# Optimization experiments

Hardware: AMD Instinct MI355X
Metric: run time of the kernel (lower is better)

## Reference

```python
import jax, jax.numpy as jnp
import numpy as np

N, E = 50000, 400000
IN_CH, HID, HEADS, EDGE_DIM = 128, 64, 4, 3
NEG_SLOPE = 0.2


def gatv2_conv(x, src, dst, edge_attr, Wl, Wr, We, att, bias):
    # x: [N, F_in]; Wl/Wr: [H*C, F_in]; We: [H*C, edge_dim]; att: [H, C]; bias: [C]
    H, C = att.shape
    n = x.shape[0]
    xl = (x @ Wl.T).reshape(n, H, C)   # source-side transform (lin_l)
    xr = (x @ Wr.T).reshape(n, H, C)   # target-side transform (lin_r)
    e = (edge_attr @ We.T).reshape(-1, H, C)
    z = jax.nn.leaky_relu(xl[src] + xr[dst] + e, NEG_SLOPE)  # [E,H,C]
    alpha = jnp.einsum('ehc,hc->eh', z, att)                 # [E,H]
    # segment softmax over incoming edges per destination node
    amax = jax.ops.segment_max(alpha, dst, num_segments=n)
    alpha = jnp.exp(alpha - amax[dst])
    denom = jax.ops.segment_sum(alpha, dst, num_segments=n)
    alpha = alpha / (denom[dst] + 1e-16)
    msg = xl[src] * alpha[:, :, None]                        # [E,H,C]
    out = jax.ops.segment_sum(msg, dst, num_segments=n)      # [N,H,C]
    return out.mean(axis=1) + bias                           # concat=False -> head mean


def setup_inputs() -> dict:
    key = jax.random.key(0)
    ks = jax.random.split(key, 16)
    s = 0.1
    return {
        'x': jax.random.normal(ks[0], (N, IN_CH), jnp.float32),
        'edge_index': jax.random.randint(ks[1], (2, E), 0, N, jnp.int32),
        'edge_attr': jax.random.normal(ks[2], (E, EDGE_DIM), jnp.float32),
        'Wl1': jax.random.normal(ks[3], (HEADS * HID, IN_CH), jnp.float32) * s,
        'Wr1': jax.random.normal(ks[4], (HEADS * HID, IN_CH), jnp.float32) * s,
        'We1': jax.random.normal(ks[5], (HEADS * HID, EDGE_DIM), jnp.float32) * s,
        'att1': jax.random.normal(ks[6], (HEADS, HID), jnp.float32) * s,
        'b1': jnp.zeros((HID,), jnp.float32),
        'Wl2': jax.random.normal(ks[7], (HEADS * HID, HID), jnp.float32) * s,
        'Wr2': jax.random.normal(ks[8], (HEADS * HID, HID), jnp.float32) * s,
        'We2': jax.random.normal(ks[9], (HEADS * HID, EDGE_DIM), jnp.float32) * s,
        'att2': jax.random.normal(ks[10], (HEADS, HID), jnp.float32) * s,
        'b2': jnp.zeros((HID,), jnp.float32),
        'prelu_w': jnp.full((HID,), 0.25, jnp.float32),
    }


def reference(x, edge_index, edge_attr, Wl1, Wr1, We1, att1, b1, Wl2, Wr2, We2, att2, b2, prelu_w):
    src, dst = edge_index[0], edge_index[1]
    h = gatv2_conv(x, src, dst, edge_attr, Wl1, Wr1, We1, att1, b1)
    h = gatv2_conv(h, src, dst, edge_attr, Wl2, Wr2, We2, att2, b2)
    return jnp.where(h >= 0, h, prelu_w * h)  # PReLU, per-channel weight
```

## Files before the change

kernel.cpp:

```cpp
#include <hip/hip_runtime.h>
#include <hip/hip_bf16.h>

#define HC 256

typedef __attribute__((ext_vector_type(8))) short bf16x8;
typedef __attribute__((ext_vector_type(4))) float f32x4;
typedef __attribute__((ext_vector_type(2))) float f32x2;

__device__ __forceinline__ void gl_lds16(const void* g, void* l) {
  __builtin_amdgcn_global_load_lds(
      (const __attribute__((address_space(1))) unsigned int*)g,
      (__attribute__((address_space(3))) unsigned int*)l, 16, 0, 0);
}

__device__ __forceinline__ void cast_w_one(const float* Wl, const float* Wr,
                                           ushort* WT, int F, int idx) {
  int col = idx / F, f = idx - col * F;
  float v = (col < 256) ? Wl[col * F + f] : Wr[(col - 256) * F + f];
  __hip_bfloat16 h = __float2bfloat16(v);
  WT[(size_t)col * F + f] = *(ushort*)&h;
}

__global__ void k_weights_deg(const float* __restrict__ Wl1, const float* __restrict__ Wr1,
                              ushort* __restrict__ WT1, const float* __restrict__ Wl2,
                              const float* __restrict__ Wr2, ushort* __restrict__ WT2,
                              int* __restrict__ deg, int n) {
  int idx = blockIdx.x * blockDim.x + threadIdx.x;
  const int t1 = 512 * 128, t2 = 512 * 64;
  if (idx < t1) {
    cast_w_one(Wl1, Wr1, WT1, 128, idx);
  } else if (idx < t1 + t2) {
    cast_w_one(Wl2, Wr2, WT2, 64, idx - t1);
  } else if (idx < t1 + t2 + n) {
    deg[idx - t1 - t2] = 0;
  }
}

template <int F>
__global__ __launch_bounds__(256) void gemm_mfma(const ushort* __restrict__ A,
                                                 const ushort* __restrict__ WT,
                                                 ushort* __restrict__ xlb,
                                                 ushort* __restrict__ xrb, int n_nodes) {
  constexpr int NSTEP = F / 64;
  __shared__ __align__(16) ushort As[128 * 64];
  __shared__ __align__(16) ushort Bs[128 * 64];
  const int tid = threadIdx.x;
  const int wv = tid >> 6, lane = tid & 63;
  const int m16 = lane & 15, quad = lane >> 4;
  const int col0 = blockIdx.x * 128;
  const int row0 = blockIdx.y * 128;
  const int wm = (wv >> 1) * 64, wn = (wv & 1) * 64;

  f32x4 acc[4][4];
#pragma unroll
  for (int i = 0; i < 4; ++i)
#pragma unroll
    for (int j = 0; j < 4; ++j) acc[i][j] = (f32x4){0.f, 0.f, 0.f, 0.f};

#pragma unroll
  for (int s = 0; s < NSTEP; ++s) {
    const int khat = s * 64;
    __syncthreads();
#pragma unroll
    for (int t = 0; t < 4; ++t) {
      const int sl16 = tid + 256 * t;
      const int row = sl16 >> 3, sl = sl16 & 7;
      const int gch = sl ^ (row & 7);
      const int grow = row0 + row;
      if (grow < n_nodes)
        gl_lds16(A + (size_t)grow * F + khat + gch * 8, As + sl16 * 8);
      gl_lds16(WT + (size_t)(col0 + row) * F + khat + gch * 8, Bs + sl16 * 8);
    }
    __syncthreads();
#pragma unroll
    for (int kh = 0; kh < 2; ++kh) {
      bf16x8 af[4], bf[4];
#pragma unroll
      for (int i = 0; i < 4; ++i) {
        const int row = wm + i * 16 + m16;
        const int slot = (kh * 4 + quad) ^ (row & 7);
        af[i] = *(bf16x8*)&As[row * 64 + slot * 8];
      }
#pragma unroll
      for (int j = 0; j < 4; ++j) {
        const int col = wn + j * 16 + m16;
        const int slot = (kh * 4 + quad) ^ (col & 7);
        bf[j] = *(bf16x8*)&Bs[col * 64 + slot * 8];
      }
#pragma unroll
      for (int i = 0; i < 4; ++i)
#pragma unroll
        for (int j = 0; j < 4; ++j)
          acc[i][j] =
              __builtin_amdgcn_mfma_f32_16x16x32_bf16(af[i], bf[j], acc[i][j], 0, 0, 0);
    }
  }
  const bool is_xl = (col0 < 256);
#pragma unroll
  for (int i = 0; i < 4; ++i) {
#pragma unroll
    for (int r = 0; r < 4; ++r) {
      const int grow = row0 + wm + i * 16 + quad * 4 + r;
      if (grow < n_nodes) {
#pragma unroll
        for (int j = 0; j < 4; ++j) {
          const float v = acc[i][j][r];
          const int col = col0 + wn + j * 16 + m16;
          __hip_bfloat16 h = __float2bfloat16(v);
          if (is_xl)
            xlb[(size_t)grow * 256 + col] = *(ushort*)&h;
          else
            xrb[(size_t)grow * 256 + (col - 256)] = *(ushort*)&h;
        }
      }
    }
  }
}

__global__ void k_hist(const int* __restrict__ ei, int* __restrict__ deg, int E_) {
  int e = blockIdx.x * blockDim.x + threadIdx.x;
  if (e < E_) atomicAdd(&deg[ei[E_ + e]], 1);
}

__global__ void k_scan_local(const int* __restrict__ deg, int* __restrict__ rowstart,
                             int* __restrict__ partial, int n) {
  __shared__ int a[256], b[256];
  const int t = threadIdx.x;
  const int i = blockIdx.x * 256 + t;
  const int v = (i < n) ? deg[i] : 0;
  a[t] = v;
  __syncthreads();
  int* cur = a;
  int* nxt = b;
  for (int off = 1; off < 256; off <<= 1) {
    int x = cur[t];
    if (t >= off) x += cur[t - off];
    nxt[t] = x;
    __syncthreads();
    int* tmp = cur; cur = nxt; nxt = tmp;
  }
  const int incl = cur[t];
  if (i < n) rowstart[i] = incl - v;
  if (t == 255) partial[blockIdx.x] = incl;
}

__global__ void k_scan_partial(int* __restrict__ partial, int nblk,
                               int* __restrict__ ssrc, float4* __restrict__ sea, int E_) {
  __shared__ int a[256], b[256];
  const int t = threadIdx.x;
  if (t < 8) {
    ssrc[E_ + t] = 0;
    sea[E_ + t] = make_float4(0.f, 0.f, 0.f, 0.f);
  }
  const int v = (t < nblk) ? partial[t] : 0;
  a[t] = v;
  __syncthreads();
  int* cur = a;
  int* nxt = b;
  for (int off = 1; off < 256; off <<= 1) {
    int x = cur[t];
    if (t >= off) x += cur[t - off];
    nxt[t] = x;
    __syncthreads();
    int* tmp = cur; cur = nxt; nxt = tmp;
  }
  if (t < nblk) partial[t] = cur[t] - v;
}

__global__ void k_add_off(int* __restrict__ rowstart, int* __restrict__ cursor,
                          const int* __restrict__ partial, int n, int E_) {
  int i = blockIdx.x * blockDim.x + threadIdx.x;
  if (i < n) {
    int v = rowstart[i] + partial[i >> 8];
    rowstart[i] = v;
    cursor[i] = v;
  }
  if (i == 0) rowstart[n] = E_;
}

__global__ void k_prep(const float* __restrict__ x, ushort* __restrict__ A,
                       const int* __restrict__ ei, const float* __restrict__ ea,
                       int* __restrict__ cursor, int* __restrict__ ssrc,
                       float4* __restrict__ sea, int n, int E_) {
  const int nx8 = n * 16;
  int idx = blockIdx.x * blockDim.x + threadIdx.x;
  if (idx < nx8) {
    const float4* xp = (const float4*)x + (size_t)idx * 2;
    float4 v0 = xp[0], v1 = xp[1];
    float vv[8] = {v0.x, v0.y, v0.z, v0.w, v1.x, v1.y, v1.z, v1.w};
    __align__(16) ushort hb[8];
#pragma unroll
    for (int j = 0; j < 8; ++j) {
      __hip_bfloat16 h = __float2bfloat16(vv[j]);
      hb[j] = *(ushort*)&h;
    }
    *(int4*)(A + (size_t)idx * 8) = *(int4*)hb;
  } else {
    int e = idx - nx8;
    if (e < E_) {
      int dst = ei[E_ + e];
      int pos = atomicAdd(&cursor[dst], 1);
      ssrc[pos] = ei[e];
      sea[pos] = make_float4(ea[e * 3], ea[e * 3 + 1], ea[e * 3 + 2], 0.f);
    }
  }
}

__device__ __forceinline__ f32x2 vmax2(f32x2 a, f32x2 b) {
  return (f32x2){fmaxf(a.x, b.x), fmaxf(a.y, b.y)};
}
__device__ __forceinline__ f32x2 vmin2(f32x2 a, f32x2 b) {
  return (f32x2){fminf(a.x, b.x), fminf(a.y, b.y)};
}

__device__ __forceinline__ void edge_step(
    const ushort4& lu, const float4& eav, const f32x2* we0, const f32x2* we1,
    const f32x2* we2, const f32x2* at, const f32x2* xrl, f32x2& num01,
    f32x2& num23, float& den) {
  f32x2 lav0, lav1;
  lav0.x = __uint_as_float((unsigned)lu.x << 16);
  lav0.y = __uint_as_float((unsigned)lu.y << 16);
  lav1.x = __uint_as_float((unsigned)lu.z << 16);
  lav1.y = __uint_as_float((unsigned)lu.w << 16);
  const f32x2 zero = {0.f, 0.f};
  const f32x2 slope = {0.2f, 0.2f};
  f32x2 pv = zero;
#pragma unroll
  for (int j = 0; j < 2; ++j) {
    f32x2 la = (j == 0) ? lav0 : lav1;
    f32x2 ev = we0[j] * eav.x + we1[j] * eav.y + we2[j] * eav.z;
    f32x2 s = la + xrl[j] + ev;
    f32x2 z = vmax2(s, zero) + slope * vmin2(s, zero);
    pv = pv + z * at[j];
  }
  float p = pv.x + pv.y;
  p += __shfl_xor(p, 1);
  p += __shfl_xor(p, 2);
  p += __shfl_xor(p, 4);
  p += __shfl_xor(p, 8);
  const float w = __expf(p);
  den += w;
  num01 = num01 + (f32x2){w, w} * lav0;
  num23 = num23 + (f32x2){w, w} * lav1;
}

template <int MODE>
__global__ __launch_bounds__(256) void fused_attn(
    const ushort* __restrict__ xlb, const ushort* __restrict__ xrb,
    const int* __restrict__ rowstart, const int* __restrict__ ssrc,
    const float4* __restrict__ sea, const float* __restrict__ We,
    const float* __restrict__ att, const float* __restrict__ bias,
    const float* __restrict__ pw, float* __restrict__ out,
    ushort* __restrict__ outs, int n, int chunk) {
  const int lane = threadIdx.x & 63;
  const int wid =
      __builtin_amdgcn_readfirstlane((blockIdx.x * blockDim.x + threadIdx.x) >> 6);
  const int d0 = wid * chunk;
  if (d0 >= n) return;
  const int d1 = min(d0 + chunk, n);

  f32x2 we0[2], we1[2], we2[2], at[2];
#pragma unroll
  for (int j = 0; j < 4; ++j) {
    int r = 4 * lane + j;
    ((float*)we0)[j] = We[r * 3 + 0];
    ((float*)we1)[j] = We[r * 3 + 1];
    ((float*)we2)[j] = We[r * 3 + 2];
    ((float*)at)[j] = att[r];
  }
  const float4 bias4 = ((const float4*)bias)[lane & 15];
  float4 pw4 = {0.f, 0.f, 0.f, 0.f};
  if (MODE == 1) pw4 = ((const float4*)pw)[lane & 15];
  const ushort4* xlb4 = (const ushort4*)xlb;

  for (int d = d0; d < d1; ++d) {
    const ushort4 xu = ((const ushort4*)xrb)[(unsigned)(d * 64) + lane];
    f32x2 xrl[2];
    xrl[0].x = __uint_as_float((unsigned)xu.x << 16);
    xrl[0].y = __uint_as_float((unsigned)xu.y << 16);
    xrl[1].x = __uint_as_float((unsigned)xu.z << 16);
    xrl[1].y = __uint_as_float((unsigned)xu.w << 16);

    int pos = rowstart[d];
    const int end = rowstart[d + 1];
    f32x2 num01 = {0.f, 0.f}, num23 = {0.f, 0.f};
    float den = 0.f;

    if (pos < end) {
      int s0 = ssrc[pos], s1 = ssrc[pos + 1];
      ushort4 g0 = xlb4[(unsigned)(s0 * 64) + lane];
      ushort4 g1 = xlb4[(unsigned)(s1 * 64) + lane];
      float4 e0 = sea[pos], e1 = sea[pos + 1];
      int sn0 = ssrc[pos + 2], sn1 = ssrc[pos + 3];

      while (pos + 2 <= end) {
        ushort4 h0 = xlb4[(unsigned)(sn0 * 64) + lane];
        ushort4 h1 = xlb4[(unsigned)(sn1 * 64) + lane];
        float4 f0 = sea[pos + 2], f1 = sea[pos + 3];
        sn0 = ssrc[pos + 4];
        sn1 = ssrc[pos + 5];
        edge_step(g0, e0, we0, we1, we2, at, xrl, num01, num23, den);
        edge_step(g1, e1, we0, we1, we2, at, xrl, num01, num23, den);
        g0 = h0; g1 = h1; e0 = f0; e1 = f1;
        pos += 2;
      }
      if (pos < end)
        edge_step(g0, e0, we0, we1, we2, at, xrl, num01, num23, den);
    }

    const float inv = 1.f / (den + 1e-16f);
    float4 r;
    r.x = num01.x * inv;
    r.y = num01.y * inv;
    r.z = num23.x * inv;
    r.w = num23.y * inv;
    r.x += __shfl_xor(r.x, 16);
    r.y += __shfl_xor(r.y, 16);
    r.z += __shfl_xor(r.z, 16);
    r.w += __shfl_xor(r.w, 16);
    r.x += __shfl_xor(r.x, 32);
    r.y += __shfl_xor(r.y, 32);
    r.z += __shfl_xor(r.z, 32);
    r.w += __shfl_xor(r.w, 32);
    if (lane < 16) {
      float o[4];
      o[0] = 0.25f * r.x + bias4.x;
      o[1] = 0.25f * r.y + bias4.y;
      o[2] = 0.25f * r.z + bias4.z;
      o[3] = 0.25f * r.w + bias4.w;
      if (MODE == 1) {
        const float pwv[4] = {pw4.x, pw4.y, pw4.z, pw4.w};
#pragma unroll
        for (int j = 0; j < 4; ++j) o[j] = (o[j] >= 0.f) ? o[j] : pwv[j] * o[j];
        ((float4*)out)[(size_t)d * 16 + lane] = make_float4(o[0], o[1], o[2], o[3]);
      } else {
        ushort hb[4];
#pragma unroll
        for (int j = 0; j < 4; ++j) {
          __hip_bfloat16 h = __float2bfloat16(o[j]);
          hb[j] = *(ushort*)&h;
        }
        *(ushort4*)(outs + (size_t)d * 64 + 4 * lane) =
            make_ushort4(hb[0], hb[1], hb[2], hb[3]);
      }
    }
  }
}

extern "C" void kernel_launch(void* const* d_in, const int* in_sizes, int n_in,
                              void* d_out, int out_size, void* d_ws, size_t ws_size,
                              hipStream_t stream) {
  const float* x    = (const float*)d_in[0];
  const int*   ei   = (const int*)d_in[1];
  const float* ea   = (const float*)d_in[2];
  const float* Wl1  = (const float*)d_in[3];
  const float* Wr1  = (const float*)d_in[4];
  const float* We1  = (const float*)d_in[5];
  const float* att1 = (const float*)d_in[6];
  const float* b1   = (const float*)d_in[7];
  const float* Wl2  = (const float*)d_in[8];
  const float* Wr2  = (const float*)d_in[9];
  const float* We2  = (const float*)d_in[10];
  const float* att2 = (const float*)d_in[11];
  const float* b2   = (const float*)d_in[12];
  const float* pw   = (const float*)d_in[13];
  const int N_ = in_sizes[0] / 128;
  const int E_ = in_sizes[1] / 2;
  float* out = (float*)d_out;

  char* w = (char*)d_ws;
  auto alloc = [&](size_t bytes) {
    char* p = w;
    w += (bytes + 255) & ~size_t(255);
    return p;
  };
  ushort* xlb      = (ushort*)alloc((size_t)N_ * 256 * 2);
  ushort* xrb      = (ushort*)alloc((size_t)N_ * 256 * 2);
  ushort* Ax       = (ushort*)alloc((size_t)N_ * 128 * 2);
  ushort* h2       = (ushort*)alloc((size_t)N_ * 64 * 2);
  int*    ssrc     = (int*)alloc((size_t)(E_ + 8) * 4);
  float4* sea      = (float4*)alloc((size_t)(E_ + 8) * 16);
  int*    deg      = (int*)alloc((size_t)N_ * 4);
  int*    rowstart = (int*)alloc((size_t)(N_ + 1) * 4);
  int*    cursor   = (int*)alloc((size_t)N_ * 4);
  int*    partial  = (int*)alloc(256 * 4);
  ushort* WT1      = (ushort*)alloc((size_t)512 * 128 * 2);
  ushort* WT2      = (ushort*)alloc((size_t)512 * 64 * 2);

  const int wtot = 512 * 128 + 512 * 64 + N_;
  k_weights_deg<<<(wtot + 255) / 256, 256, 0, stream>>>(Wl1, Wr1, WT1, Wl2, Wr2, WT2,
                                                        deg, N_);

  const int nblk = (N_ + 255) / 256;
  k_hist<<<(E_ + 255) / 256, 256, 0, stream>>>(ei, deg, E_);
  k_scan_local<<<nblk, 256, 0, stream>>>(deg, rowstart, partial, N_);
  k_scan_partial<<<1, 256, 0, stream>>>(partial, nblk, ssrc, sea, E_);
  k_add_off<<<nblk, 256, 0, stream>>>(rowstart, cursor, partial, N_, E_);
  const int ptot = N_ * 16 + E_;
  k_prep<<<(ptot + 255) / 256, 256, 0, stream>>>(x, Ax, ei, ea, cursor, ssrc, sea,
                                                 N_, E_);

  const dim3 GG(4, (N_ + 127) / 128);
  const int FW = 8192;
  const int FB = FW / 4;
  const int chunk = (N_ + FW - 1) / FW;

  gemm_mfma<128><<<GG, 256, 0, stream>>>(Ax, WT1, xlb, xrb, N_);
  fused_attn<0><<<FB, 256, 0, stream>>>(xlb, xrb, rowstart, ssrc, sea, We1, att1,
                                        b1, pw, nullptr, h2, N_, chunk);
  gemm_mfma<64><<<GG, 256, 0, stream>>>(h2, WT2, xlb, xrb, N_);
  fused_attn<1><<<FB, 256, 0, stream>>>(xlb, xrb, rowstart, ssrc, sea, We2, att2,
                                        b2, pw, out, nullptr, N_, chunk);
}
```

Baseline: 280.3 us.

## Unroll edge gather to four-way prefetch, fuse histogram into weight cast, shrink node chunk

```diff
diff --git a/kernel.cpp b/kernel.cpp
--- a/kernel.cpp
+++ b/kernel.cpp
@@ -21,18 +21,19 @@
   WT[(size_t)col * F + f] = *(ushort*)&h;
 }
 
-__global__ void k_weights_deg(const float* __restrict__ Wl1, const float* __restrict__ Wr1,
-                              ushort* __restrict__ WT1, const float* __restrict__ Wl2,
-                              const float* __restrict__ Wr2, ushort* __restrict__ WT2,
-                              int* __restrict__ deg, int n) {
+__global__ void k_weights_hist(const float* __restrict__ Wl1, const float* __restrict__ Wr1,
+                               ushort* __restrict__ WT1, const float* __restrict__ Wl2,
+                               const float* __restrict__ Wr2, ushort* __restrict__ WT2,
+                               const int* __restrict__ ei, int* __restrict__ deg, int E_) {
   int idx = blockIdx.x * blockDim.x + threadIdx.x;
   const int t1 = 512 * 128, t2 = 512 * 64;
   if (idx < t1) {
     cast_w_one(Wl1, Wr1, WT1, 128, idx);
   } else if (idx < t1 + t2) {
     cast_w_one(Wl2, Wr2, WT2, 64, idx - t1);
-  } else if (idx < t1 + t2 + n) {
-    deg[idx - t1 - t2] = 0;
+  } else {
+    int e = idx - t1 - t2;
+    if (e < E_) atomicAdd(&deg[ei[E_ + e]], 1);
   }
 }
 
@@ -115,11 +116,6 @@
       }
     }
   }
-}
-
-__global__ void k_hist(const int* __restrict__ ei, int* __restrict__ deg, int E_) {
-  int e = blockIdx.x * blockDim.x + threadIdx.x;
-  if (e < E_) atomicAdd(&deg[ei[E_ + e]], 1);
 }
 
 __global__ void k_scan_local(const int* __restrict__ deg, int* __restrict__ rowstart,
@@ -287,25 +283,40 @@
     float den = 0.f;
 
     if (pos < end) {
-      int s0 = ssrc[pos], s1 = ssrc[pos + 1];
+      int s0 = ssrc[pos], s1 = ssrc[pos + 1], s2 = ssrc[pos + 2], s3 = ssrc[pos + 3];
       ushort4 g0 = xlb4[(unsigned)(s0 * 64) + lane];
       ushort4 g1 = xlb4[(unsigned)(s1 * 64) + lane];
-      float4 e0 = sea[pos], e1 = sea[pos + 1];
-      int sn0 = ssrc[pos + 2], sn1 = ssrc[pos + 3];
-
-      while (pos + 2 <= end) {
-        ushort4 h0 = xlb4[(unsigned)(sn0 * 64) + lane];
-        ushort4 h1 = xlb4[(unsigned)(sn1 * 64) + lane];
-        float4 f0 = sea[pos + 2], f1 = sea[pos + 3];
-        sn0 = ssrc[pos + 4];
-        sn1 = ssrc[pos + 5];
+      ushort4 g2 = xlb4[(unsigned)(s2 * 64) + lane];
+      ushort4 g3 = xlb4[(unsigned)(s3 * 64) + lane];
+      float4 e0 = sea[pos], e1 = sea[pos + 1], e2 = sea[pos + 2], e3 = sea[pos + 3];
+
+      while (pos + 4 <= end) {
+        ushort4 h0 = g0, h1 = g1, h2 = g2, h3 = g3;
+        float4 f0 = e0, f1 = e1, f2 = e2, f3 = e3;
+        if (pos + 4 < end) {
+          int t0 = ssrc[pos + 4], t1 = ssrc[pos + 5], t2 = ssrc[pos + 6],
+              t3 = ssrc[pos + 7];
+          h0 = xlb4[(unsigned)(t0 * 64) + lane];
+          h1 = xlb4[(unsigned)(t1 * 64) + lane];
+          h2 = xlb4[(unsigned)(t2 * 64) + lane];
+          h3 = xlb4[(unsigned)(t3 * 64) + lane];
+          f0 = sea[pos + 4];
+          f1 = sea[pos + 5];
+          f2 = sea[pos + 6];
+          f3 = sea[pos + 7];
+        }
         edge_step(g0, e0, we0, we1, we2, at, xrl, num01, num23, den);
         edge_step(g1, e1, we0, we1, we2, at, xrl, num01, num23, den);
-        g0 = h0; g1 = h1; e0 = f0; e1 = f1;
-        pos += 2;
+        edge_step(g2, e2, we0, we1, we2, at, xrl, num01, num23, den);
+        edge_step(g3, e3, we0, we1, we2, at, xrl, num01, num23, den);
+        g0 = h0; g1 = h1; g2 = h2; g3 = h3;
+        e0 = f0; e1 = f1; e2 = f2; e3 = f3;
+        pos += 4;
       }
-      if (pos < end)
-        edge_step(g0, e0, we0, we1, we2, at, xrl, num01, num23, den);
+      const int rem = end - pos;
+      if (rem > 0) edge_step(g0, e0, we0, we1, we2, at, xrl, num01, num23, den);
+      if (rem > 1) edge_step(g1, e1, we0, we1, we2, at, xrl, num01, num23, den);
+      if (rem > 2) edge_step(g2, e2, we0, we1, we2, at, xrl, num01, num23, den);
     }
 
     const float inv = 1.f / (den + 1e-16f);
@@ -387,12 +398,12 @@
   ushort* WT1      = (ushort*)alloc((size_t)512 * 128 * 2);
   ushort* WT2      = (ushort*)alloc((size_t)512 * 64 * 2);
 
-  const int wtot = 512 * 128 + 512 * 64 + N_;
-  k_weights_deg<<<(wtot + 255) / 256, 256, 0, stream>>>(Wl1, Wr1, WT1, Wl2, Wr2, WT2,
-                                                        deg, N_);
+  hipMemsetAsync(deg, 0, (size_t)N_ * 4, stream);
+  const int wtot = 512 * 128 + 512 * 64 + E_;
+  k_weights_hist<<<(wtot + 255) / 256, 256, 0, stream>>>(Wl1, Wr1, WT1, Wl2, Wr2, WT2,
+                                                         ei, deg, E_);
 
   const int nblk = (N_ + 255) / 256;
-  k_hist<<<(E_ + 255) / 256, 256, 0, stream>>>(ei, deg, E_);
   k_scan_local<<<nblk, 256, 0, stream>>>(deg, rowstart, partial, N_);
   k_scan_partial<<<1, 256, 0, stream>>>(partial, nblk, ssrc, sea, E_);
   k_add_off<<<nblk, 256, 0, stream>>>(rowstart, cursor, partial, N_, E_);
@@ -401,9 +412,9 @@
                                                  N_, E_);
 
   const dim3 GG(4, (N_ + 127) / 128);
-  const int FW = 8192;
-  const int FB = FW / 4;
-  const int chunk = (N_ + FW - 1) / FW;
+  const int chunk = 2;
+  const int nwav = (N_ + chunk - 1) / chunk;
+  const int FB = (nwav + 3) / 4;
 
   gemm_mfma<128><<<GG, 256, 0, stream>>>(Ax, WT1, xlb, xrb, N_);
   fused_attn<0><<<FB, 256, 0, stream>>>(xlb, xrb, rowstart, ssrc, sea, We1, att1,
```

Measured after the change: 282.3 us. About the same (+0.7%).
